# Kernel optimization log

Measured on AMD Instinct MI355X. Metric: run time of the kernel, lower is better.

The kernel has to match this reference:

```python
import jax, jax.numpy as jnp
import numpy as np

MODEL = 2048
LATENT = 512
POS = 1024
NH = 16
HD = MODEL // NH        # 128
PHD = POS // NH         # 64
THETA = 50000.0


def _rope_tables(S, dim, base=THETA):
    inv_freq = 1.0 / (base ** (jnp.arange(0, dim, 2, dtype=jnp.float32) / dim))
    t = jnp.arange(S, dtype=jnp.float32)
    freqs = jnp.outer(t, inv_freq)                  # [S, dim/2]
    emb = jnp.concatenate([freqs, freqs], axis=-1)  # [S, dim]
    return jnp.cos(emb), jnp.sin(emb)


def _rotate_half(x):
    h = x.shape[-1] // 2
    return jnp.concatenate([-x[..., h:], x[..., :h]], axis=-1)


def _apply_rope(x, cos, sin):
    # x: [..., S, dim]; cos/sin: [S, dim]
    return x * cos + _rotate_half(x) * sin


def setup_inputs() -> dict:
    key = jax.random.key(0)
    ks = jax.random.split(key, 16)
    std = 0.02
    d = {
        'x':      jax.random.normal(ks[0], (2, 2048, MODEL), jnp.float32),
        'w_qkv':  jax.random.normal(ks[1], (MODEL, 3 * LATENT), jnp.float32) * std,
        'b_qkv':  jnp.zeros((3 * LATENT,), jnp.float32),
        'w_qup':  jax.random.normal(ks[2], (LATENT, MODEL), jnp.float32) * std,
        'b_qup':  jnp.zeros((MODEL,), jnp.float32),
        'w_kup':  jax.random.normal(ks[3], (LATENT, MODEL), jnp.float32) * std,
        'b_kup':  jnp.zeros((MODEL,), jnp.float32),
        'w_vup':  jax.random.normal(ks[4], (LATENT, MODEL), jnp.float32) * std,
        'b_vup':  jnp.zeros((MODEL,), jnp.float32),
        'w_qpos': jax.random.normal(ks[5], (LATENT, POS), jnp.float32) * std,
        'b_qpos': jnp.zeros((POS,), jnp.float32),
        'w_kpos': jax.random.normal(ks[6], (MODEL, PHD), jnp.float32) * std,
        'b_kpos': jnp.zeros((PHD,), jnp.float32),
        'w_o':    jax.random.normal(ks[7], (MODEL, MODEL), jnp.float32) * std,
        'b_o':    jnp.zeros((MODEL,), jnp.float32),
    }
    return d


def reference(x, w_qkv, b_qkv, w_qup, b_qup, w_kup, b_kup, w_vup, b_vup,
              w_qpos, b_qpos, w_kpos, b_kpos, w_o, b_o):
    B, S, _ = x.shape
    # fused down-projection into shared latent
    latent_qkv = x @ w_qkv + b_qkv                       # [B,S,3L]
    lq, lk, lv = jnp.split(latent_qkv, 3, axis=-1)       # each [B,S,L]

    cos, sin = _rope_tables(S, PHD)

    # decoupled positional key (shared across heads), RoPE on sub-slice
    pos_k = x @ w_kpos + b_kpos                          # [B,S,PHD]
    pos_k = _apply_rope(pos_k, cos, sin)

    # up-projections
    q = (lq @ w_qup + b_qup).reshape(B, S, NH, HD).transpose(0, 2, 1, 3)
    k = (lk @ w_kup + b_kup).reshape(B, S, NH, HD).transpose(0, 2, 1, 3)
    v = (lv @ w_vup + b_vup).reshape(B, S, NH, HD).transpose(0, 2, 1, 3)

    pos_q = (lq @ w_qpos + b_qpos).reshape(B, S, NH, PHD).transpose(0, 2, 1, 3)
    pos_q = _apply_rope(pos_q, cos, sin)                 # [B,NH,S,PHD]

    pos_kh = jnp.broadcast_to(pos_k[:, None], (B, NH, S, PHD))
    q = jnp.concatenate([q, pos_q], axis=-1)             # [B,NH,S,HD+PHD]
    k = jnp.concatenate([k, pos_kh], axis=-1)

    scale = 1.0 / jnp.sqrt(jnp.asarray(HD + PHD, x.dtype))
    scores = jnp.einsum('bhqd,bhkd->bhqk', q, k) * scale
    causal = jnp.tril(jnp.ones((S, S), bool))
    scores = jnp.where(causal, scores, jnp.finfo(scores.dtype).min)
    p = jax.nn.softmax(scores, axis=-1)
    attn = jnp.einsum('bhqk,bhkd->bhqd', p, v)           # [B,NH,S,HD]
    attn = attn.transpose(0, 2, 1, 3).reshape(B, S, MODEL)
    return attn @ w_o + b_o
```

## Files before the change

kernel.cpp:

```cpp
#include <hip/hip_runtime.h>
#include <cstdint>
#include <cstddef>

typedef __bf16 bf16x8 __attribute__((ext_vector_type(8)));
typedef float  f32x4  __attribute__((ext_vector_type(4)));
typedef unsigned short us8 __attribute__((ext_vector_type(8)));
typedef unsigned short us4 __attribute__((ext_vector_type(4)));

__device__ __forceinline__ unsigned short f2bf(float f) {
  union { float f; unsigned u; } v; v.f = f;
  unsigned r = v.u + 0x7FFFu + ((v.u >> 16) & 1u);
  return (unsigned short)(r >> 16);
}
__device__ __forceinline__ float b2f(unsigned short h) {
  union { unsigned u; float f; } v; v.u = ((unsigned)h) << 16;
  return v.f;
}
__device__ __forceinline__ f32x4 mfma16(bf16x8 a, bf16x8 b, f32x4 c) {
  return __builtin_amdgcn_mfma_f32_16x16x32_bf16(a, b, c, 0, 0, 0);
}
__device__ __forceinline__ void gl_lds16(const unsigned short* g, unsigned short* l) {
  __builtin_amdgcn_global_load_lds(
      (const __attribute__((address_space(1))) void*)g,
      (__attribute__((address_space(3))) void*)l, 16, 0, 0);
}

__global__ void prep_misc_kernel(const float* __restrict__ b_qkv,
                                 const float* __restrict__ b_kpos,
                                 const float* __restrict__ b_qup,
                                 const float* __restrict__ b_qpos,
                                 float* __restrict__ bias1,
                                 float* __restrict__ bias2q,
                                 float* __restrict__ costab,
                                 float* __restrict__ sintab,
                                 unsigned short* __restrict__ wB1pad) {
  int i = blockIdx.x * 256 + threadIdx.x;
  if (i < 65536) {
    int s = i >> 5, f = i & 31;
    float inv = powf(50000.0f, -(float)f / 32.0f);
    float a = (float)s * inv;
    costab[i] = cosf(a);
    sintab[i] = sinf(a);
  }
  if (i < 1664) bias1[i] = (i < 1536) ? b_qkv[i] : (i < 1600 ? b_kpos[i - 1536] : 0.0f);
  if (i < 3072) bias2q[i] = (i < 2048) ? b_qup[i] : b_qpos[i - 2048];
  if (i < 131072) wB1pad[i] = 0;
}

__global__ void convx_kernel(const float* __restrict__ in,
                             unsigned short* __restrict__ out, int n4) {
  int i = blockIdx.x * 256 + threadIdx.x;
  if (i < n4) {
    float4 v = ((const float4*)in)[i];
    us4 o;
    o[0] = f2bf(v.x); o[1] = f2bf(v.y); o[2] = f2bf(v.z); o[3] = f2bf(v.w);
    ((us4*)out)[i] = o;
  }
}

__global__ void tconv_kernel(const float* __restrict__ in, int ldin,
                             unsigned short* __restrict__ out, int ldo) {
  __shared__ float tile[32][33];
  int c0 = blockIdx.x * 32, r0 = blockIdx.y * 32;
  int tx = threadIdx.x & 31, ty = threadIdx.x >> 5;
  for (int j = 0; j < 4; ++j)
    tile[ty + j * 8][tx] = in[(size_t)(r0 + ty + j * 8) * ldin + c0 + tx];
  __syncthreads();
  for (int j = 0; j < 4; ++j)
    out[(size_t)(c0 + ty + j * 8) * ldo + r0 + tx] = f2bf(tile[tx][ty + j * 8]);
}

template <int OUT_MODE>
__global__ __launch_bounds__(256, 2)
void gemm_bt_kernel(const unsigned short* __restrict__ A, int lda,
                    const unsigned short* __restrict__ Bt, int ldb,
                    void* __restrict__ Cout, int ldc,
                    const float* __restrict__ bias, int K) {
  __shared__ unsigned short smem[32768];
  int tid = threadIdx.x;
  int wave = tid >> 6, lane = tid & 63;
  int g = lane >> 4, r = lane & 15;
  int wr = wave >> 1, wc = wave & 1;
  long brow = (long)blockIdx.y * 128, bcol = (long)blockIdx.x * 128;

  int srowl = lane >> 3;
  int sw = ((lane & 7) ^ (srowl & 7)) * 8;
  const unsigned short* Abase = A + (brow + wave * 32 + srowl) * (long)lda + sw;
  const unsigned short* Bbase = Bt + (bcol + wave * 32 + srowl) * (long)ldb + sw;

  f32x4 acc[4][4];
  for (int mi = 0; mi < 4; ++mi)
    for (int ni = 0; ni < 4; ++ni)
      acc[mi][ni] = f32x4{0.f, 0.f, 0.f, 0.f};

  auto stage = [&](int buf, int k0) {
    unsigned short* ab = smem + buf * 16384;
    unsigned short* bb = ab + 8192;
    for (int c = 0; c < 4; ++c) {
      gl_lds16(Abase + (size_t)c * 8 * lda + k0, ab + (wave * 32 + c * 8) * 64);
      gl_lds16(Bbase + (size_t)c * 8 * ldb + k0, bb + (wave * 32 + c * 8) * 64);
    }
  };

  int rx = (r & 7) << 4;
  int nt = K >> 6;

  stage(0, 0);
  for (int t = 0; t < nt; ++t) {
    if (t + 1 < nt) {
      stage((t + 1) & 1, (t + 1) << 6);
      asm volatile("s_waitcnt vmcnt(8)" ::: "memory");
    } else {
      asm volatile("s_waitcnt vmcnt(0)" ::: "memory");
    }
    __builtin_amdgcn_sched_barrier(0);
    __builtin_amdgcn_s_barrier();
    __builtin_amdgcn_sched_barrier(0);
    const char* Ab = (const char*)(smem + (t & 1) * 16384);
    const char* Bb = Ab + 16384;
    for (int kk = 0; kk < 2; ++kk) {
      bf16x8 af[4], bfv[4];
      for (int mi = 0; mi < 4; ++mi)
        af[mi] = *(const bf16x8*)(Ab + (size_t)(wr * 64 + mi * 16 + r) * 128 +
                                  ((kk * 64 + g * 16) ^ rx));
      for (int ni = 0; ni < 4; ++ni)
        bfv[ni] = *(const bf16x8*)(Bb + (size_t)(wc * 64 + ni * 16 + r) * 128 +
                                   ((kk * 64 + g * 16) ^ rx));
      for (int mi = 0; mi < 4; ++mi)
        for (int ni = 0; ni < 4; ++ni)
          acc[mi][ni] = mfma16(af[mi], bfv[ni], acc[mi][ni]);
    }
    __builtin_amdgcn_sched_barrier(0);
    __builtin_amdgcn_s_barrier();
  }

  if (OUT_MODE == 2) {
    for (int mi = 0; mi < 4; ++mi)
      for (int ni = 0; ni < 4; ++ni) {
        int col = wc * 64 + ni * 16 + r;
        float bv = bias[bcol + col];
        int rowb = wr * 64 + mi * 16 + g * 4;
        for (int i = 0; i < 4; ++i)
          smem[col * 136 + rowb + i] = f2bf(acc[mi][ni][i] + bv);
      }
    __syncthreads();
    int col = tid >> 1, half = tid & 1;
    int bh = (int)(brow >> 11) * 16 + (int)(bcol >> 7);
    unsigned short* outp = (unsigned short*)Cout +
                           ((size_t)bh * 128 + col) * 2048 + (brow & 2047);
    for (int j = 0; j < 8; ++j) {
      int row0 = half * 64 + j * 8;
      *(us8*)(outp + row0) = *(const us8*)&smem[col * 136 + row0];
    }
    return;
  }

  for (int mi = 0; mi < 4; ++mi)
    for (int ni = 0; ni < 4; ++ni) {
      long col = bcol + wc * 64 + ni * 16 + r;
      float bv = bias ? bias[col] : 0.0f;
      long rowb = brow + wr * 64 + mi * 16 + g * 4;
      for (int i = 0; i < 4; ++i) {
        float v = acc[mi][ni][i] + bv;
        if (OUT_MODE == 1)
          ((float*)Cout)[(rowb + i) * (long)ldc + col] = v;
        else
          ((unsigned short*)Cout)[(rowb + i) * (long)ldc + col] = f2bf(v);
      }
    }
}

__global__ void rope_kernel(const unsigned short* __restrict__ tmp_q,
                            const unsigned short* __restrict__ latext,
                            const float* __restrict__ costab,
                            const float* __restrict__ sintab,
                            unsigned short* __restrict__ posqr,
                            unsigned short* __restrict__ poskr) {
  int idx = blockIdx.x * 256 + threadIdx.x;
  const unsigned short* src;
  unsigned short* dst;
  int s, dp0;
  if (idx < 524288) {
    int rowA = idx >> 7, rem = idx & 127;
    int h = rem >> 3;
    dp0 = (rem & 7) * 8;
    s = rowA & 2047;
    src = tmp_q + (size_t)rowA * 3072 + 2048 + h * 64;
    dst = posqr + (size_t)rowA * 1024 + h * 64 + dp0;
  } else if (idx < 557056) {
    int j = idx - 524288;
    int rowA = j >> 3;
    dp0 = (j & 7) * 8;
    s = rowA & 2047;
    src = latext + (size_t)rowA * 1664 + 1536;
    dst = poskr + (size_t)rowA * 64 + dp0;
  } else {
    return;
  }
  us8 x1 = *(const us8*)(src + dp0);
  us8 x2 = *(const us8*)(src + (dp0 ^ 32));
  int f0 = dp0 & 31;
  const float* cp = costab + s * 32 + f0;
  const float* sp = sintab + s * 32 + f0;
  bool low = dp0 < 32;
  us8 o;
  for (int e = 0; e < 8; ++e) {
    float a = b2f(x1[e]), b = b2f(x2[e]);
    float v = low ? (a * cp[e] - b * sp[e]) : (a * cp[e] + b * sp[e]);
    o[e] = f2bf(v);
  }
  *(us8*)dst = o;
}

__device__ __forceinline__ void task_decode(int t, int& qt, int& seg, int& bh) {
  if (t < 1024) {
    qt = 31 - (t >> 7); int rem = t & 127; seg = rem >> 5; bh = rem & 31;
  } else if (t < 1792) {
    int t2 = t - 1024; int qi = t2 / 96; int rem = t2 - qi * 96;
    qt = 23 - qi; seg = rem >> 5; bh = rem & 31;
  } else if (t < 2304) {
    int t3 = t - 1792; qt = 15 - (t3 >> 6); int rem = t3 & 63; seg = rem >> 5; bh = rem & 31;
  } else {
    int t4 = t - 2304; qt = 7 - (t4 >> 5); seg = 0; bh = t4 & 31;
  }
}
__device__ __forceinline__ int task_slot(int qt, int seg, int bh) {
  if (qt >= 24) return (31 - qt) * 128 + seg * 32 + bh;
  if (qt >= 16) return 1024 + (23 - qt) * 96 + seg * 32 + bh;
  return 1792 + (15 - qt) * 64 + seg * 32 + bh;
}

__global__ __launch_bounds__(256, 2)
void flash_kernel(const unsigned short* __restrict__ tmp_q,
                  const unsigned short* __restrict__ tmp_k,
                  const unsigned short* __restrict__ posqr,
                  const unsigned short* __restrict__ poskr,
                  const unsigned short* __restrict__ vT,
                  unsigned short* __restrict__ ob,
                  unsigned short* __restrict__ Opart,
                  float* __restrict__ mlbuf,
                  int* __restrict__ counter) {
  const int S = 2048;
  int tid = threadIdx.x, wave = tid >> 6, lane = tid & 63;
  int g = lane >> 4, r = lane & 15;
  const float sl2 = 1.44269504f / 13.8564064605510183f;
  const float DEFER = 96.0f;

  __shared__ unsigned short Klds[32 * 192];
  __shared__ unsigned short Vlds[128 * 32];
  __shared__ unsigned short Plds[4][16][40];
  __shared__ int s_tile;
  char* Kb = (char*)Klds;
  char* Vb = (char*)Vlds;
  int rx7 = (r & 7) << 4, rx3 = (r & 3) << 4;

  us8 onesu;
  for (int e = 0; e < 8; ++e) onesu[e] = 0x3F80;
  bf16x8 ones = *(const bf16x8*)&onesu;

  int kn_row[2], kn_seg[2];
  for (int j = 0; j < 2; ++j) {
    int slot = j * 256 + tid;
    kn_row[j] = slot >> 4;
    kn_seg[j] = slot & 15;
  }
  int kr_row = tid >> 3, kr_seg = tid & 7;
  int v_row[2], v_seg[2];
  for (int j = 0; j < 2; ++j) {
    int slot = j * 256 + tid;
    v_row[j] = slot >> 2;
    v_seg[j] = slot & 3;
  }

  for (;;) {
    if (tid == 0) s_tile = atomicAdd(counter, 1);
    __syncthreads();
    int t = s_tile;
    if (t >= 2560) return;
    int qt, seg, bh;
    task_decode(t, qt, seg, bh);
    int b = bh >> 4, h = bh & 15;
    int qbase = qt * 64;
    int cbeg = seg * 16;
    int cend = min(cbeg + 16, 2 * (qt + 1));
    size_t rb = (size_t)b * 2048;

    const unsigned short* kpn = tmp_k + rb * 2048 + h * 128;
    const unsigned short* kpr = poskr + rb * 64;
    const unsigned short* vp = vT + (size_t)bh * 128 * S;

    bf16x8 qf[6];
    {
      size_t qrowA = rb + qbase + wave * 16 + r;
      const unsigned short* qn = tmp_q + qrowA * 3072 + h * 128 + g * 8;
      for (int c = 0; c < 4; ++c) qf[c] = *(const bf16x8*)(qn + c * 32);
      const unsigned short* qr_ = posqr + qrowA * 1024 + h * 64 + g * 8;
      qf[4] = *(const bf16x8*)(qr_);
      qf[5] = *(const bf16x8*)(qr_ + 32);
    }

    f32x4 acc[8];
    for (int d = 0; d < 8; ++d) acc[d] = f32x4{0.f, 0.f, 0.f, 0.f};
    f32x4 lacc = {0.f, 0.f, 0.f, 0.f};
    float m_r[4];
    for (int i = 0; i < 4; ++i) m_r[i] = -3.0e38f;

    us8 kreg[2], krope, vreg[2];
    {
      int kv0 = cbeg * 32;
      for (int j = 0; j < 2; ++j)
        kreg[j] = *(const us8*)(kpn + (size_t)(kv0 + kn_row[j]) * 2048 + kn_seg[j] * 8);
      krope = *(const us8*)(kpr + (size_t)(kv0 + kr_row) * 64 + kr_seg * 8);
      for (int j = 0; j < 2; ++j)
        vreg[j] = *(const us8*)(vp + (size_t)v_row[j] * S + kv0 + v_seg[j] * 8);
    }

    for (int ch = cbeg; ch < cend; ++ch) {
      for (int j = 0; j < 2; ++j)
        *(us8*)(Kb + (size_t)kn_row[j] * 384 +
                ((kn_seg[j] ^ (kn_row[j] & 7)) << 4)) = kreg[j];
      *(us8*)(Kb + (size_t)kr_row * 384 +
              (((16 + kr_seg) ^ (kr_row & 7)) << 4)) = krope;
      for (int j = 0; j < 2; ++j)
        *(us8*)(Vb + (size_t)v_row[j] * 64 +
                ((v_seg[j] ^ (v_row[j] & 3)) << 4)) = vreg[j];
      asm volatile("s_waitcnt lgkmcnt(0)" ::: "memory");
      __builtin_amdgcn_sched_barrier(0);
      __builtin_amdgcn_s_barrier();
      __builtin_amdgcn_sched_barrier(0);
      if (ch + 1 < cend) {
        int kv1 = (ch + 1) * 32;
        for (int j = 0; j < 2; ++j)
          kreg[j] = *(const us8*)(kpn + (size_t)(kv1 + kn_row[j]) * 2048 + kn_seg[j] * 8);
        krope = *(const us8*)(kpr + (size_t)(kv1 + kr_row) * 64 + kr_seg * 8);
        for (int j = 0; j < 2; ++j)
          vreg[j] = *(const us8*)(vp + (size_t)v_row[j] * S + kv1 + v_seg[j] * 8);
      }
      int kv0 = ch * 32;

      f32x4 sc0 = {0.f, 0.f, 0.f, 0.f}, sc1 = {0.f, 0.f, 0.f, 0.f};
      __builtin_amdgcn_s_setprio(1);
      for (int c = 0; c < 6; ++c) {
        bf16x8 kf0 = *(const bf16x8*)(Kb + (size_t)r * 384 + (((c * 4 + g) << 4) ^ rx7));
        sc0 = mfma16(qf[c], kf0, sc0);
      }
      for (int c = 0; c < 6; ++c) {
        bf16x8 kf1 = *(const bf16x8*)(Kb + (size_t)(16 + r) * 384 + (((c * 4 + g) << 4) ^ rx7));
        sc1 = mfma16(qf[c], kf1, sc1);
      }
      __builtin_amdgcn_s_setprio(0);

      int kj0 = kv0 + r, kj1 = kv0 + 16 + r;
      int qi0 = qbase + wave * 16 + g * 4;
      for (int i = 0; i < 4; ++i) {
        if (kj0 > qi0 + i) sc0[i] = -1e30f;
        if (kj1 > qi0 + i) sc1[i] = -1e30f;
      }

      float tl[4];
      bool ok = true;
      for (int i = 0; i < 4; ++i) {
        tl[i] = fmaxf(sc0[i], sc1[i]);
        ok = ok && (tl[i] - m_r[i] <= DEFER);
      }
      if (!__all(ok)) {
        for (int i = 0; i < 4; ++i) {
          float tm = tl[i];
          for (int off = 1; off < 16; off <<= 1) tm = fmaxf(tm, __shfl_xor(tm, off, 64));
          float mnew = fmaxf(m_r[i], tm);
          float corr = exp2f((m_r[i] - mnew) * sl2);
          lacc[i] *= corr;
          for (int d = 0; d < 8; ++d) acc[d][i] *= corr;
          m_r[i] = mnew;
        }
      }
      float p0[4], p1[4];
      for (int i = 0; i < 4; ++i) {
        p0[i] = exp2f((sc0[i] - m_r[i]) * sl2);
        p1[i] = exp2f((sc1[i] - m_r[i]) * sl2);
      }

      for (int i = 0; i < 4; ++i) {
        Plds[wave][g * 4 + i][r] = f2bf(p0[i]);
        Plds[wave][g * 4 + i][16 + r] = f2bf(p1[i]);
      }
      bf16x8 pa = *(const bf16x8*)&Plds[wave][r][g * 8];
      __builtin_amdgcn_s_setprio(1);
      lacc = mfma16(pa, ones, lacc);
      for (int dt = 0; dt < 8; ++dt) {
        bf16x8 vf = *(const bf16x8*)(Vb + (size_t)(dt * 16 + r) * 64 + ((g << 4) ^ rx3));
        acc[dt] = mfma16(pa, vf, acc[dt]);
      }
      __builtin_amdgcn_s_setprio(0);
      __builtin_amdgcn_sched_barrier(0);
      __builtin_amdgcn_s_barrier();
    }

    if (qt <= 7) {
      for (int i = 0; i < 4; ++i) {
        float inv = 1.0f / lacc[i];
        int row = qbase + wave * 16 + g * 4 + i;
        size_t base = (rb + row) * 2048 + h * 128;
        for (int dt = 0; dt < 8; ++dt)
          ob[base + dt * 16 + r] = f2bf(acc[dt][i] * inv);
      }
    } else {
      unsigned short* op = Opart + (size_t)t * 8192;
      for (int i = 0; i < 4; ++i) {
        int row = wave * 16 + g * 4 + i;
        for (int dt = 0; dt < 8; ++dt)
          op[row * 128 + dt * 16 + r] = f2bf(acc[dt][i]);
        if (r == 0) {
          mlbuf[(size_t)t * 128 + row * 2]     = m_r[i];
          mlbuf[(size_t)t * 128 + row * 2 + 1] = lacc[i];
        }
      }
    }
  }
}

__global__ void merge_kernel(const unsigned short* __restrict__ Opart,
                             const float* __restrict__ mlbuf,
                             unsigned short* __restrict__ ob) {
  int qt = 8 + (blockIdx.x >> 5), bh = blockIdx.x & 31;
  int b = bh >> 4, h = bh & 15;
  int tid = threadIdx.x;
  int row = tid >> 2, c0 = (tid & 3) * 32;
  const float sl2 = 1.44269504f / 13.8564064605510183f;
  int ns = (qt >= 24) ? 4 : (qt >= 16 ? 3 : 2);

  size_t slot[4];
  float m[4], l[4], w[4];
  float M = -3.0e38f;
#pragma unroll
  for (int j = 0; j < 4; ++j) {
    if (j < ns) {
      slot[j] = task_slot(qt, j, bh);
      m[j] = mlbuf[slot[j] * 128 + row * 2];
      l[j] = mlbuf[slot[j] * 128 + row * 2 + 1];
      M = fmaxf(M, m[j]);
    }
  }
  float L = 0.f;
#pragma unroll
  for (int j = 0; j < 4; ++j)
    if (j < ns) { w[j] = exp2f((m[j] - M) * sl2); L += w[j] * l[j]; }
  float invL = 1.f / L;
#pragma unroll
  for (int j = 0; j < 4; ++j) if (j < ns) w[j] *= invL;

  float o[32];
#pragma unroll
  for (int e = 0; e < 32; ++e) o[e] = 0.f;
#pragma unroll
  for (int j = 0; j < 4; ++j) {
    if (j < ns) {
      const unsigned short* pp = Opart + slot[j] * 8192 + row * 128 + c0;
      for (int blk = 0; blk < 4; ++blk) {
        us8 v = *(const us8*)(pp + blk * 8);
        for (int e = 0; e < 8; ++e) o[blk * 8 + e] += w[j] * b2f(v[e]);
      }
    }
  }
  size_t obase = ((size_t)b * 2048 + qt * 64 + row) * 2048 + h * 128 + c0;
  for (int blk = 0; blk < 4; ++blk) {
    us8 st;
    for (int e = 0; e < 8; ++e) st[e] = f2bf(o[blk * 8 + e]);
    *(us8*)(ob + obase + blk * 8) = st;
  }
}

extern "C" void kernel_launch(void* const* d_in, const int* in_sizes, int n_in,
                              void* d_out, int out_size, void* d_ws, size_t ws_size,
                              hipStream_t stream) {
  const float* x      = (const float*)d_in[0];
  const float* w_qkv  = (const float*)d_in[1];
  const float* b_qkv  = (const float*)d_in[2];
  const float* w_qup  = (const float*)d_in[3];
  const float* b_qup  = (const float*)d_in[4];
  const float* w_kup  = (const float*)d_in[5];
  const float* b_kup  = (const float*)d_in[6];
  const float* w_vup  = (const float*)d_in[7];
  const float* b_vup  = (const float*)d_in[8];
  const float* w_qpos = (const float*)d_in[9];
  const float* b_qpos = (const float*)d_in[10];
  const float* w_kpos = (const float*)d_in[11];
  const float* b_kpos = (const float*)d_in[12];
  const float* w_o    = (const float*)d_in[13];
  const float* b_o    = (const float*)d_in[14];
  (void)in_sizes; (void)n_in; (void)out_size; (void)ws_size;

  char* ws = (char*)d_ws;
  size_t off = 0;
  auto alloc = [&](size_t bytes) -> char* {
    char* p = ws + off;
    off += (bytes + 255) & ~(size_t)255;
    return p;
  };

  unsigned short* xb     = (unsigned short*)alloc(16777216);
  unsigned short* wB1    = (unsigned short*)alloc(6815744);
  unsigned short* wB2q   = (unsigned short*)alloc(3145728);
  unsigned short* wB2k   = (unsigned short*)alloc(2097152);
  unsigned short* wB2v   = (unsigned short*)alloc(2097152);
  unsigned short* wBo    = (unsigned short*)alloc(8388608);
  float*          bias1  = (float*)alloc(1664 * 4);
  float*          bias2q = (float*)alloc(3072 * 4);
  float*          costab = (float*)alloc(262144);
  float*          sintab = (float*)alloc(262144);
  unsigned short* latext = (unsigned short*)alloc(13631488);
  unsigned short* tmp_q  = (unsigned short*)alloc(25165824);
  unsigned short* tmp_k  = (unsigned short*)alloc(16777216);
  unsigned short* vTbuf  = (unsigned short*)alloc(16777216);
  unsigned short* posqr  = (unsigned short*)alloc(8388608);
  unsigned short* poskr  = (unsigned short*)alloc(524288);
  unsigned short* Opart  = (unsigned short*)alloc(41943040);
  float*          mlbuf  = (float*)alloc(1310720);
  int*            counter= (int*)alloc(256);
  unsigned short* attnb  = xb;

  prep_misc_kernel<<<512, 256, 0, stream>>>(b_qkv, b_kpos, b_qup, b_qpos,
                                            bias1, bias2q, costab, sintab,
                                            wB1 + (size_t)1600 * 2048);
  convx_kernel<<<8192, 256, 0, stream>>>(x, xb, 2097152);
  tconv_kernel<<<dim3(48, 64), 256, 0, stream>>>(w_qkv, 1536, wB1, 2048);
  tconv_kernel<<<dim3(2, 64), 256, 0, stream>>>(w_kpos, 64, wB1 + (size_t)1536 * 2048, 2048);
  tconv_kernel<<<dim3(64, 16), 256, 0, stream>>>(w_qup, 2048, wB2q, 512);
  tconv_kernel<<<dim3(32, 16), 256, 0, stream>>>(w_qpos, 1024, wB2q + (size_t)2048 * 512, 512);
  tconv_kernel<<<dim3(64, 16), 256, 0, stream>>>(w_kup, 2048, wB2k, 512);
  tconv_kernel<<<dim3(64, 16), 256, 0, stream>>>(w_vup, 2048, wB2v, 512);
  tconv_kernel<<<dim3(64, 64), 256, 0, stream>>>(w_o, 2048, wBo, 2048);

  gemm_bt_kernel<0><<<dim3(13, 32), 256, 0, stream>>>(xb, 2048, wB1, 2048,
                                                      latext, 1664, bias1, 2048);
  gemm_bt_kernel<0><<<dim3(24, 32), 256, 0, stream>>>(latext, 1664, wB2q, 512,
                                                      tmp_q, 3072, bias2q, 512);
  gemm_bt_kernel<0><<<dim3(16, 32), 256, 0, stream>>>(latext + 512, 1664, wB2k, 512,
                                                      tmp_k, 2048, b_kup, 512);
  gemm_bt_kernel<2><<<dim3(16, 32), 256, 0, stream>>>(latext + 1024, 1664, wB2v, 512,
                                                      vTbuf, 2048, b_vup, 512);
  rope_kernel<<<2176, 256, 0, stream>>>(tmp_q, latext, costab, sintab, posqr, poskr);
  hipMemsetAsync(counter, 0, 4, stream);
  flash_kernel<<<1024, 256, 0, stream>>>(tmp_q, tmp_k, posqr, poskr, vTbuf,
                                         attnb, Opart, mlbuf, counter);
  merge_kernel<<<768, 256, 0, stream>>>(Opart, mlbuf, attnb);
  gemm_bt_kernel<1><<<dim3(16, 32), 256, 0, stream>>>(attnb, 2048, wBo, 2048,
                                                      d_out, 2048, b_o, 2048);
}
```

Before: 295.9 us.

## Double flash attention query tile to 128 rows with 512-thread blocks

```diff
diff --git a/kernel.cpp b/kernel.cpp
--- a/kernel.cpp
+++ b/kernel.cpp
@@ -213,24 +213,23 @@
 }
 
 __device__ __forceinline__ void task_decode(int t, int& qt, int& seg, int& bh) {
-  if (t < 1024) {
-    qt = 31 - (t >> 7); int rem = t & 127; seg = rem >> 5; bh = rem & 31;
-  } else if (t < 1792) {
-    int t2 = t - 1024; int qi = t2 / 96; int rem = t2 - qi * 96;
-    qt = 23 - qi; seg = rem >> 5; bh = rem & 31;
-  } else if (t < 2304) {
-    int t3 = t - 1792; qt = 15 - (t3 >> 6); int rem = t3 & 63; seg = rem >> 5; bh = rem & 31;
+  if (t < 512) { qt = 15 - (t >> 7); seg = (t >> 5) & 3; bh = t & 31; }
+  else if (t < 896) {
+    int t2 = t - 512; int qi = t2 / 96;
+    qt = 11 - qi; seg = (t2 - qi * 96) >> 5; bh = t2 & 31;
+  } else if (t < 1152) {
+    int t3 = t - 896; qt = 7 - (t3 >> 6); seg = (t3 >> 5) & 1; bh = t3 & 31;
   } else {
-    int t4 = t - 2304; qt = 7 - (t4 >> 5); seg = 0; bh = t4 & 31;
+    int t4 = t - 1152; qt = 3 - (t4 >> 5); seg = 0; bh = t4 & 31;
   }
 }
 __device__ __forceinline__ int task_slot(int qt, int seg, int bh) {
-  if (qt >= 24) return (31 - qt) * 128 + seg * 32 + bh;
-  if (qt >= 16) return 1024 + (23 - qt) * 96 + seg * 32 + bh;
-  return 1792 + (15 - qt) * 64 + seg * 32 + bh;
-}
-
-__global__ __launch_bounds__(256, 2)
+  if (qt >= 12) return (15 - qt) * 128 + seg * 32 + bh;
+  if (qt >= 8)  return 512 + (11 - qt) * 96 + seg * 32 + bh;
+  return 896 + (7 - qt) * 64 + seg * 32 + bh;
+}
+
+__global__ __launch_bounds__(512, 2)
 void flash_kernel(const unsigned short* __restrict__ tmp_q,
                   const unsigned short* __restrict__ tmp_k,
                   const unsigned short* __restrict__ posqr,
@@ -248,7 +247,7 @@
 
   __shared__ unsigned short Klds[32 * 192];
   __shared__ unsigned short Vlds[128 * 32];
-  __shared__ unsigned short Plds[4][16][40];
+  __shared__ unsigned short Plds[8][16][40];
   __shared__ int s_tile;
   char* Kb = (char*)Klds;
   char* Vb = (char*)Vlds;
@@ -258,31 +257,21 @@
   for (int e = 0; e < 8; ++e) onesu[e] = 0x3F80;
   bf16x8 ones = *(const bf16x8*)&onesu;
 
-  int kn_row[2], kn_seg[2];
-  for (int j = 0; j < 2; ++j) {
-    int slot = j * 256 + tid;
-    kn_row[j] = slot >> 4;
-    kn_seg[j] = slot & 15;
-  }
-  int kr_row = tid >> 3, kr_seg = tid & 7;
-  int v_row[2], v_seg[2];
-  for (int j = 0; j < 2; ++j) {
-    int slot = j * 256 + tid;
-    v_row[j] = slot >> 2;
-    v_seg[j] = slot & 3;
-  }
+  int kn_row = tid >> 4, kn_seg = tid & 15;
+  int kr_row = (tid & 255) >> 3, kr_seg = tid & 7;
+  int v_row = tid >> 2, v_seg = tid & 3;
 
   for (;;) {
     if (tid == 0) s_tile = atomicAdd(counter, 1);
     __syncthreads();
     int t = s_tile;
-    if (t >= 2560) return;
+    if (t >= 1280) return;
     int qt, seg, bh;
     task_decode(t, qt, seg, bh);
     int b = bh >> 4, h = bh & 15;
-    int qbase = qt * 64;
+    int qbase = qt * 128;
     int cbeg = seg * 16;
-    int cend = min(cbeg + 16, 2 * (qt + 1));
+    int cend = min(cbeg + 16, 4 * (qt + 1));
     size_t rb = (size_t)b * 2048;
 
     const unsigned short* kpn = tmp_k + rb * 2048 + h * 128;
@@ -305,36 +294,30 @@
     float m_r[4];
     for (int i = 0; i < 4; ++i) m_r[i] = -3.0e38f;
 
-    us8 kreg[2], krope, vreg[2];
+    us8 kreg, krope, vreg;
     {
       int kv0 = cbeg * 32;
-      for (int j = 0; j < 2; ++j)
-        kreg[j] = *(const us8*)(kpn + (size_t)(kv0 + kn_row[j]) * 2048 + kn_seg[j] * 8);
-      krope = *(const us8*)(kpr + (size_t)(kv0 + kr_row) * 64 + kr_seg * 8);
-      for (int j = 0; j < 2; ++j)
-        vreg[j] = *(const us8*)(vp + (size_t)v_row[j] * S + kv0 + v_seg[j] * 8);
+      kreg = *(const us8*)(kpn + (size_t)(kv0 + kn_row) * 2048 + kn_seg * 8);
+      if (tid < 256)
+        krope = *(const us8*)(kpr + (size_t)(kv0 + kr_row) * 64 + kr_seg * 8);
+      vreg = *(const us8*)(vp + (size_t)v_row * S + kv0 + v_seg * 8);
     }
 
     for (int ch = cbeg; ch < cend; ++ch) {
-      for (int j = 0; j < 2; ++j)
-        *(us8*)(Kb + (size_t)kn_row[j] * 384 +
-                ((kn_seg[j] ^ (kn_row[j] & 7)) << 4)) = kreg[j];
-      *(us8*)(Kb + (size_t)kr_row * 384 +
-              (((16 + kr_seg) ^ (kr_row & 7)) << 4)) = krope;
-      for (int j = 0; j < 2; ++j)
-        *(us8*)(Vb + (size_t)v_row[j] * 64 +
-                ((v_seg[j] ^ (v_row[j] & 3)) << 4)) = vreg[j];
+      *(us8*)(Kb + (size_t)kn_row * 384 + ((kn_seg ^ (kn_row & 7)) << 4)) = kreg;
+      if (tid < 256)
+        *(us8*)(Kb + (size_t)kr_row * 384 + (((16 + kr_seg) ^ (kr_row & 7)) << 4)) = krope;
+      *(us8*)(Vb + (size_t)v_row * 64 + ((v_seg ^ (v_row & 3)) << 4)) = vreg;
       asm volatile("s_waitcnt lgkmcnt(0)" ::: "memory");
       __builtin_amdgcn_sched_barrier(0);
       __builtin_amdgcn_s_barrier();
       __builtin_amdgcn_sched_barrier(0);
       if (ch + 1 < cend) {
         int kv1 = (ch + 1) * 32;
-        for (int j = 0; j < 2; ++j)
-          kreg[j] = *(const us8*)(kpn + (size_t)(kv1 + kn_row[j]) * 2048 + kn_seg[j] * 8);
-        krope = *(const us8*)(kpr + (size_t)(kv1 + kr_row) * 64 + kr_seg * 8);
-        for (int j = 0; j < 2; ++j)
-          vreg[j] = *(const us8*)(vp + (size_t)v_row[j] * S + kv1 + v_seg[j] * 8);
+        kreg = *(const us8*)(kpn + (size_t)(kv1 + kn_row) * 2048 + kn_seg * 8);
+        if (tid < 256)
+          krope = *(const us8*)(kpr + (size_t)(kv1 + kr_row) * 64 + kr_seg * 8);
+        vreg = *(const us8*)(vp + (size_t)v_row * S + kv1 + v_seg * 8);
       }
       int kv0 = ch * 32;
 
@@ -350,11 +333,14 @@
       }
       __builtin_amdgcn_s_setprio(0);
 
-      int kj0 = kv0 + r, kj1 = kv0 + 16 + r;
-      int qi0 = qbase + wave * 16 + g * 4;
-      for (int i = 0; i < 4; ++i) {
-        if (kj0 > qi0 + i) sc0[i] = -1e30f;
-        if (kj1 > qi0 + i) sc1[i] = -1e30f;
+      int qi_min = qbase + wave * 16;
+      if (kv0 + 31 > qi_min) {
+        int kj0 = kv0 + r, kj1 = kv0 + 16 + r;
+        int qi0 = qi_min + g * 4;
+        for (int i = 0; i < 4; ++i) {
+          if (kj0 > qi0 + i) sc0[i] = -1e30f;
+          if (kj1 > qi0 + i) sc1[i] = -1e30f;
+        }
       }
 
       float tl[4];
@@ -396,7 +382,7 @@
       __builtin_amdgcn_s_barrier();
     }
 
-    if (qt <= 7) {
+    if (qt <= 3) {
       for (int i = 0; i < 4; ++i) {
         float inv = 1.0f / lacc[i];
         int row = qbase + wave * 16 + g * 4 + i;
@@ -405,14 +391,14 @@
           ob[base + dt * 16 + r] = f2bf(acc[dt][i] * inv);
       }
     } else {
-      unsigned short* op = Opart + (size_t)t * 8192;
+      unsigned short* op = Opart + (size_t)t * 16384;
       for (int i = 0; i < 4; ++i) {
         int row = wave * 16 + g * 4 + i;
         for (int dt = 0; dt < 8; ++dt)
           op[row * 128 + dt * 16 + r] = f2bf(acc[dt][i]);
         if (r == 0) {
-          mlbuf[(size_t)t * 128 + row * 2]     = m_r[i];
-          mlbuf[(size_t)t * 128 + row * 2 + 1] = lacc[i];
+          mlbuf[(size_t)t * 256 + row * 2]     = m_r[i];
+          mlbuf[(size_t)t * 256 + row * 2 + 1] = lacc[i];
         }
       }
     }
@@ -422,12 +408,12 @@
 __global__ void merge_kernel(const unsigned short* __restrict__ Opart,
                              const float* __restrict__ mlbuf,
                              unsigned short* __restrict__ ob) {
-  int qt = 8 + (blockIdx.x >> 5), bh = blockIdx.x & 31;
+  int qt = 4 + (blockIdx.x >> 5), bh = blockIdx.x & 31;
   int b = bh >> 4, h = bh & 15;
   int tid = threadIdx.x;
-  int row = tid >> 2, c0 = (tid & 3) * 32;
+  int row = tid >> 1, half = (tid & 1) * 64;
   const float sl2 = 1.44269504f / 13.8564064605510183f;
-  int ns = (qt >= 24) ? 4 : (qt >= 16 ? 3 : 2);
+  int ns = (qt >= 12) ? 4 : (qt >= 8 ? 3 : 2);
 
   size_t slot[4];
   float m[4], l[4], w[4];
@@ -436,8 +422,8 @@
   for (int j = 0; j < 4; ++j) {
     if (j < ns) {
       slot[j] = task_slot(qt, j, bh);
-      m[j] = mlbuf[slot[j] * 128 + row * 2];
-      l[j] = mlbuf[slot[j] * 128 + row * 2 + 1];
+      m[j] = mlbuf[slot[j] * 256 + row * 2];
+      l[j] = mlbuf[slot[j] * 256 + row * 2 + 1];
       M = fmaxf(M, m[j]);
     }
   }
@@ -449,21 +435,21 @@
 #pragma unroll
   for (int j = 0; j < 4; ++j) if (j < ns) w[j] *= invL;
 
-  float o[32];
+  float o[64];
 #pragma unroll
-  for (int e = 0; e < 32; ++e) o[e] = 0.f;
+  for (int e = 0; e < 64; ++e) o[e] = 0.f;
 #pragma unroll
   for (int j = 0; j < 4; ++j) {
     if (j < ns) {
-      const unsigned short* pp = Opart + slot[j] * 8192 + row * 128 + c0;
-      for (int blk = 0; blk < 4; ++blk) {
+      const unsigned short* pp = Opart + slot[j] * 16384 + row * 128 + half;
+      for (int blk = 0; blk < 8; ++blk) {
         us8 v = *(const us8*)(pp + blk * 8);
         for (int e = 0; e < 8; ++e) o[blk * 8 + e] += w[j] * b2f(v[e]);
       }
     }
   }
-  size_t obase = ((size_t)b * 2048 + qt * 64 + row) * 2048 + h * 128 + c0;
-  for (int blk = 0; blk < 4; ++blk) {
+  size_t obase = ((size_t)b * 2048 + qt * 128 + row) * 2048 + h * 128 + half;
+  for (int blk = 0; blk < 8; ++blk) {
     us8 st;
     for (int e = 0; e < 8; ++e) st[e] = f2bf(o[blk * 8 + e]);
     *(us8*)(ob + obase + blk * 8) = st;
@@ -514,7 +500,7 @@
   unsigned short* vTbuf  = (unsigned short*)alloc(16777216);
   unsigned short* posqr  = (unsigned short*)alloc(8388608);
   unsigned short* poskr  = (unsigned short*)alloc(524288);
-  unsigned short* Opart  = (unsigned short*)alloc(41943040);
+  unsigned short* Opart  = (unsigned short*)alloc(37748736);
   float*          mlbuf  = (float*)alloc(1310720);
   int*            counter= (int*)alloc(256);
   unsigned short* attnb  = xb;
@@ -541,9 +527,9 @@
                                                       vTbuf, 2048, b_vup, 512);
   rope_kernel<<<2176, 256, 0, stream>>>(tmp_q, latext, costab, sintab, posqr, poskr);
   hipMemsetAsync(counter, 0, 4, stream);
-  flash_kernel<<<1024, 256, 0, stream>>>(tmp_q, tmp_k, posqr, poskr, vTbuf,
-                                         attnb, Opart, mlbuf, counter);
-  merge_kernel<<<768, 256, 0, stream>>>(Opart, mlbuf, attnb);
+  flash_kernel<<<768, 512, 0, stream>>>(tmp_q, tmp_k, posqr, poskr, vTbuf,
+                                        attnb, Opart, mlbuf, counter);
+  merge_kernel<<<384, 256, 0, stream>>>(Opart, mlbuf, attnb);
   gemm_bt_kernel<1><<<dim3(16, 32), 256, 0, stream>>>(attnb, 2048, wBo, 2048,
                                                       d_out, 2048, b_o, 2048);
 }
```

Result: slower. 307.4 us (+3.9%).
